# Kernel tuning notes

Measured on AMD Instinct MI355X. Metric: run time of the kernel, lower is better.

The kernel has to match this reference:

```python
import jax, jax.numpy as jnp
from jax import lax
import numpy as np

K = 2000      # self.k: entries kept per sample
T_SC = 3      # number of IHT iterations
DN = ('NCHW', 'OIHW', 'NCHW')


def keep_k_largest(X, k):
    # Per-sample hard threshold: keep the k largest-magnitude entries of the
    # flattened [C,H,W] activations, zero the rest (exactly k kept, as in argsort).
    B = X.shape[0]
    flat = X.reshape(B, -1)                                # [B, N]
    _, idx = lax.top_k(jnp.abs(flat), k)                   # [B, k]
    vals = jnp.take_along_axis(flat, idx, axis=1)          # [B, k]
    out = jnp.zeros_like(flat).at[jnp.arange(B)[:, None], idx].set(vals)
    return out.reshape(X.shape)


def _D_apply(X, W_D):
    # ConvTranspose2d(numb_atom -> dp_channels), stride 1, no padding:
    # full correlation with the spatially flipped, io-swapped kernel.
    kh, kw = W_D.shape[2], W_D.shape[3]
    Wt = jnp.flip(jnp.transpose(W_D, (1, 0, 2, 3)), (2, 3))  # [dp, atoms, kh, kw]
    return lax.conv_general_dilated(X, Wt, (1, 1),
                                    [(kh - 1, kh - 1), (kw - 1, kw - 1)],
                                    dimension_numbers=DN)


def _Dt_apply(Z, W_D):
    # Conv2d(dp_channels -> numb_atom) VALID; D_trans.weight = D.weight.permute(0,1,3,2)
    Wt = jnp.transpose(W_D, (0, 1, 3, 2))                  # [atoms, dp, kh, kw]
    return lax.conv_general_dilated(Z, Wt, (1, 1), 'VALID', dimension_numbers=DN)


def setup_inputs() -> dict:
    key = jax.random.key(0)
    k1, k2, k3 = jax.random.split(key, 3)
    Y = jax.random.normal(k1, (32, 3, 64, 64), jnp.float32)
    X0 = jax.random.normal(k2, (32, 128, 57, 57), jnp.float32)   # random init X in forward
    W_D = jax.random.normal(k3, (128, 3, 8, 8), jnp.float32) * 0.05
    return {"Y": Y, "X0": X0, "W_D": W_D}


def reference(Y, X0, W_D):
    # HT_arg = X - D_trans(D(X) - Y); then T_SC hard-threshold iterations.
    HT_arg = X0 - _Dt_apply(_D_apply(X0, W_D) - Y, W_D)
    X = HT_arg
    for i in range(T_SC):
        X = keep_k_largest(HT_arg, K)
        if i < T_SC - 1:  # final HT_arg update in the original is unused
            HT_arg = X - _Dt_apply(_D_apply(X, W_D) - Y, W_D)
    return X
```

## Files before the change

### kernel.cpp

```cpp
#include <hip/hip_runtime.h>

#define BATCH 32
#define ATOMS 128
#define CCH 3
#define XH 57
#define XW 57
#define OHH 64
#define OWW 64
#define KSEL 2000
#define PIX (XH*XW)
#define NPS (ATOMS*PIX)
#define NTOT (BATCH*NPS)
#define RPS (CCH*OHH*OWW)
#define RTOT (BATCH*RPS)
#define CANDCAP 32768
#define NW 24576
#define ZWORDS (32*2048 + 32*1024)

__global__ __launch_bounds__(256) void prep_k(const float* __restrict__ Wg,
    double* __restrict__ WDd, double* __restrict__ Wt2d,
    const float* __restrict__ Y, double* __restrict__ Rd,
    unsigned* __restrict__ zbuf) {
  int e = blockIdx.x * 256 + threadIdx.x;
  if (e < NW) {
    {
      int kw = e & 7; int t = e >> 3; int c = t % 3; t /= 3; int kh = t & 7; int a = t >> 3;
      WDd[e] = (double)Wg[(a*3 + c)*64 + kh*8 + kw];
    }
    {
      int a = e & 127; int t = e >> 7; int j = t & 7; int i = (t >> 3) & 7; int c = t >> 6;
      Wt2d[e] = (double)Wg[(a*3 + c)*64 + j*8 + i];
    }
  }
  if (e < RTOT) Rd[e] = -(double)Y[e];
  if (e < ZWORDS + 64) zbuf[e] = 0;
}

__global__ __launch_bounds__(256) void convD_k(const float* __restrict__ X,
    const double* __restrict__ WDd, double* __restrict__ Rd) {
  __shared__ double Xs[4][11][72];
  int p = blockIdx.x;
  int lg = (p & 7) * 256 + (p >> 3);
  int b = lg >> 6; int rem = lg & 63;
  int band = rem >> 2, quarter = rem & 3;
  int row0 = band * 4;
  int a_base = quarter * 32;
  int tid = threadIdx.x;
  int ox = tid & 63;
  int wv = __builtin_amdgcn_readfirstlane(tid >> 6);
  const float* Xb = X + (size_t)b * NPS;

  double acc[4][3];
#pragma unroll
  for (int ty = 0; ty < 4; ++ty)
#pragma unroll
    for (int c = 0; c < 3; ++c) acc[ty][c] = 0.0;

  for (int ch = 0; ch < 8; ++ch) {
    __syncthreads();
    for (int e = tid; e < 4 * 11 * 72; e += 256) {
      int ai = e / 792; int rem2 = e - ai * 792;
      int r = rem2 / 72; int ss = rem2 - r * 72;
      int gy = row0 - 7 + r;
      int xcol = ss - 7;
      int a = a_base + ch * 4 + ai;
      float v = 0.0f;
      if ((unsigned)xcol < (unsigned)XW && (unsigned)gy < (unsigned)XH)
        v = Xb[a * PIX + gy * XW + xcol];
      Xs[ai][r][ss] = (double)v;
    }
    __syncthreads();
    {
      int a = a_base + ch * 4 + wv;
      const double* Wa = WDd + a * 192;
#pragma unroll
      for (int r = 0; r < 11; ++r) {
        int gy = row0 - 7 + r;
        if ((unsigned)gy >= (unsigned)XH) continue;
        double xd[8];
#pragma unroll
        for (int t = 0; t < 8; ++t) xd[t] = Xs[wv][r][ox + t];
#pragma unroll
        for (int ty = 0; ty < 4; ++ty) {
          int kh = ty + 7 - r;
          if ((unsigned)kh < 8u) {
            const double* Wk = Wa + kh * 24;
#pragma unroll
            for (int kw = 0; kw < 8; ++kw) {
              acc[ty][0] = fma(xd[7 - kw], Wk[kw],      acc[ty][0]);
              acc[ty][1] = fma(xd[7 - kw], Wk[8 + kw],  acc[ty][1]);
              acc[ty][2] = fma(xd[7 - kw], Wk[16 + kw], acc[ty][2]);
            }
          }
        }
      }
    }
  }
#pragma unroll
  for (int ty = 0; ty < 4; ++ty) {
    int oy = row0 + ty;
#pragma unroll
    for (int c = 0; c < 3; ++c)
      atomicAdd(&Rd[((size_t)(b * CCH + c) << 12) + (oy << 6) + ox], acc[ty][c]);
  }
}

__global__ __launch_bounds__(256) void convD_sparse_k(const float* __restrict__ Wg,
    const int* __restrict__ nzidx, const float* __restrict__ nzval,
    const float* __restrict__ Y, float* __restrict__ R) {
  __shared__ double accd[512];
  __shared__ float Wf[8192];
  __shared__ int   li[KSEL];
  __shared__ float lv[KSEL];
  int p = blockIdx.x;
  int lg = (p & 7) * 96 + (p >> 3);
  int s = lg / 24; int r = lg % 24; int c = r >> 3; int band = r & 7;
  int row0 = band * 8;
  int tid = threadIdx.x;
  for (int e = tid; e < 512; e += 256) accd[e] = 0.0;
  for (int e = tid; e < 8192; e += 256) {
    int a = e >> 6, k2 = e & 63;
    Wf[e] = Wg[(a * 3 + c) * 64 + k2];
  }
  for (int e = tid; e < KSEL; e += 256) {
    li[e] = nzidx[s * KSEL + e];
    lv[e] = nzval[s * KSEL + e];
  }
  __syncthreads();
  int slot = tid >> 3, kw = tid & 7;
  for (int e = slot; e < KSEL; e += 32) {
    int idx = li[e];
    int a = (int)((unsigned)idx / 3249u);
    int pp = idx - a * 3249;
    int y = (int)((unsigned)pp / 57u);
    int x = pp - y * 57;
    int dy = y - row0;
    if (dy < -7 || dy > 7) continue;
    double val = (double)lv[e];
    const float* wp = Wf + (a << 6) + kw;
#pragma unroll
    for (int kh = 0; kh < 8; ++kh) {
      int rr = dy + kh;
      if ((unsigned)rr < 8u)
        __hip_atomic_fetch_add(&accd[(rr << 6) + x + kw],
                               val * (double)wp[kh << 3],
                               __ATOMIC_RELAXED, __HIP_MEMORY_SCOPE_WORKGROUP);
    }
  }
  __syncthreads();
  const float* Yb = Y + (((size_t)(s * CCH + c)) << 12) + (row0 << 6);
  float* Rb = R + (((size_t)(s * CCH + c)) << 12) + (row0 << 6);
  for (int e = tid; e < 512; e += 256)
    Rb[e] = (float)(accd[e] - (double)Yb[e]);
}

template <typename TR>
__global__ __launch_bounds__(256) void convDt_k(const TR* __restrict__ R,
    const double* __restrict__ Wt2d, const float* __restrict__ Xprev,
    float* __restrict__ HT, unsigned* __restrict__ g1) {
  __shared__ float Rl[3][15][72];
  __shared__ unsigned hh[1024];
  int p = blockIdx.x;
  int lg = (p & 7) * 512 + (p >> 3);
  int b = lg >> 7; int rem = lg & 127; int ag = rem >> 3; int by = rem & 7;
  int row0 = by * 8;
  int a0 = ag * 8;
  int tid = threadIdx.x;
  for (int e = tid; e < 1024; e += 256) hh[e] = 0;
  for (int e = tid; e < 3 * 15 * 72; e += 256) {
    int c = e / (15 * 72); int r2 = e - c * (15 * 72);
    int rr = r2 / 72; int cc = r2 - rr * 72;
    int gr = row0 + rr;
    float v = 0.0f;
    if (cc < OWW && gr < OHH)
      v = (float)R[((size_t)(b * CCH + c) << 12) + (gr << 6) + cc];
    Rl[c][rr][cc] = v;
  }
  __syncthreads();
  int x = tid & 63, yg = tid >> 6;
  int yb = yg * 2;
  double acc[8][2];
#pragma unroll
  for (int aa = 0; aa < 8; ++aa) { acc[aa][0] = 0.0; acc[aa][1] = 0.0; }

#pragma unroll 1
  for (int c = 0; c < 3; ++c) {
#pragma unroll 1
    for (int j = 0; j < 8; ++j) {
      double rw[9];
#pragma unroll
      for (int r = 0; r < 9; ++r) rw[r] = (double)Rl[c][yb + r][x + j];
#pragma unroll
      for (int i = 0; i < 8; ++i) {
        const double* wp = Wt2d + ((c * 8 + i) * 8 + j) * 128 + a0;
#pragma unroll
        for (int aa = 0; aa < 8; ++aa) {
          double w = wp[aa];
          acc[aa][0] = fma(rw[i + 0], w, acc[aa][0]);
          acc[aa][1] = fma(rw[i + 1], w, acc[aa][1]);
        }
      }
    }
  }
  if (x < XW) {
#pragma unroll
    for (int ty = 0; ty < 2; ++ty) {
      int yy = row0 + yb + ty;
      if (yy < XH) {
#pragma unroll
        for (int aa = 0; aa < 8; ++aa) {
          size_t xo = (size_t)(b * ATOMS + a0 + aa) * PIX + yy * XW + x;
          float fv = (float)((double)Xprev[xo] - acc[aa][ty]);
          HT[xo] = fv;
          unsigned u = __float_as_uint(fv) & 0x7fffffffu;
          unsigned bin = u >> 20;
          atomicAdd(&hh[bin >> 1], 1u << ((bin & 1) << 4));
        }
      }
    }
  }
  __syncthreads();
  unsigned* gp = g1 + (size_t)b * 2048;
  for (int e = tid; e < 1024; e += 256) {
    unsigned v = hh[e];
    unsigned lo = v & 0xffffu, hi = v >> 16;
    if (lo) atomicAdd(&gp[2 * e], lo);
    if (hi) atomicAdd(&gp[2 * e + 1], hi);
  }
}

__global__ __launch_bounds__(256) void histwrite_k(const float* __restrict__ HT,
    const unsigned* __restrict__ g1, unsigned* __restrict__ g2,
    int* __restrict__ cand, int* __restrict__ candcnt,
    float* __restrict__ Xo, int* __restrict__ nzidx, float* __restrict__ nzval,
    int* __restrict__ nzcnt, int emit) {
  __shared__ unsigned h[1024];
  __shared__ unsigned part[256];
  __shared__ int lidx[4096];
  __shared__ int kidx[2048];
  __shared__ float kval[2048];
  __shared__ int lcnt, lbase, kcnt, kbase, b1_sh;
  int tid = threadIdx.x;
  int s = blockIdx.x >> 5;
  int chunk = blockIdx.x & 31;
  const unsigned* hg1 = g1 + (size_t)s * 2048;
  unsigned psum = 0;
#pragma unroll
  for (int e = 0; e < 8; ++e) psum += hg1[tid * 8 + e];
  part[tid] = psum;
  for (int e = tid; e < 1024; e += 256) h[e] = 0;
  if (tid == 0) { lcnt = 0; kcnt = 0; }
  __syncthreads();
  if (tid == 0) {
    int Kv = KSEL;
    unsigned cumBefore = 0;
    int bsel = 0;
    for (int q = 255; q >= 0; --q) {
      unsigned ps = part[q];
      if ((int)(cumBefore + ps) >= Kv) {
        for (int e = q * 8 + 7;; --e) {
          unsigned c2 = cumBefore + hg1[e];
          if ((int)c2 >= Kv) { bsel = e; break; }
          cumBefore = c2;
        }
        break;
      }
      cumBefore += ps;
    }
    b1_sh = bsel;
  }
  __syncthreads();
  unsigned pre = (unsigned)b1_sh;
  size_t sbase = (size_t)s * NPS;
  const uint4* U4 = (const uint4*)(HT + sbase);
  float4* X4 = (float4*)(Xo + sbase);
  for (int i4 = chunk * 256 + tid; i4 < NPS / 4; i4 += 32 * 256) {
    uint4 v = U4[i4];
    unsigned uu[4] = {v.x, v.y, v.z, v.w};
    float oo[4];
#pragma unroll
    for (int t = 0; t < 4; ++t) {
      int il = i4 * 4 + t;
      unsigned u = uu[t] & 0x7fffffffu;
      unsigned bin = u >> 20;
      float val = __uint_as_float(uu[t]);
      if (bin > pre) {
        oo[t] = val;
        if (emit) {
          int pos = atomicAdd(&kcnt, 1);
          if (pos < 2048) { kidx[pos] = il; kval[pos] = val; }
        }
      } else if (bin < pre) {
        oo[t] = 0.0f;
      } else {
        oo[t] = val;
        atomicAdd(&h[(u >> 10) & 1023], 1u);
        int pos = atomicAdd(&lcnt, 1);
        if (pos < 4096) lidx[pos] = il;
      }
    }
    X4[i4] = make_float4(oo[0], oo[1], oo[2], oo[3]);
  }
  __syncthreads();
  if (tid == 0) {
    int n = lcnt < 4096 ? lcnt : 4096;
    lbase = atomicAdd(&candcnt[s], n);
    if (emit) {
      int kn = kcnt < 2048 ? kcnt : 2048;
      kbase = atomicAdd(&nzcnt[s], kn);
    }
  }
  __syncthreads();
  int n = lcnt < 4096 ? lcnt : 4096;
  for (int e = tid; e < n; e += 256) {
    int g = lbase + e;
    if (g < CANDCAP) cand[s * CANDCAP + g] = lidx[e];
  }
  if (emit) {
    int kn = kcnt < 2048 ? kcnt : 2048;
    for (int e = tid; e < kn; e += 256) {
      int g = kbase + e;
      if (g < KSEL) { nzidx[s * KSEL + g] = kidx[e]; nzval[s * KSEL + g] = kval[e]; }
    }
  }
  for (int e = tid; e < 1024; e += 256)
    if (h[e]) atomicAdd(&g2[s * 1024 + e], h[e]);
}

__global__ __launch_bounds__(256) void pass3_k(const float* __restrict__ HT,
    const int* __restrict__ cand, int* __restrict__ candcnt,
    unsigned* __restrict__ g1, unsigned* __restrict__ g2,
    float* __restrict__ Xo, int* __restrict__ nzidx, float* __restrict__ nzval,
    int* __restrict__ nzcnt, int emit) {
  int s = blockIdx.x;
  __shared__ unsigned h[1024];
  __shared__ unsigned part[256];
  __shared__ int eqidx[1024];
  __shared__ int kidx[2048];
  __shared__ float kval[2048];
  __shared__ int eqn, kcnt, kbase;
  __shared__ unsigned tau_sh;
  __shared__ int k3_sh, cutoff_sh;
  __shared__ int b1_sh, k1_sh, b2_sh, k2_sh;
  int t = threadIdx.x;
  unsigned* hg1 = g1 + (size_t)s * 2048;
  unsigned s1 = 0;
#pragma unroll
  for (int e = 0; e < 8; ++e) s1 += hg1[t * 8 + e];
  part[t] = s1;
  for (int e = t; e < 1024; e += 256) h[e] = 0;
  if (t == 0) { eqn = 0; kcnt = 0; }
  __syncthreads();
  if (t == 0) {
    int Kv = KSEL;
    unsigned cumBefore = 0;
    int bsel = 0;
    for (int q = 255; q >= 0; --q) {
      unsigned ps = part[q];
      if ((int)(cumBefore + ps) >= Kv) {
        for (int e = q * 8 + 7;; --e) {
          unsigned c2 = cumBefore + hg1[e];
          if ((int)c2 >= Kv) { bsel = e; break; }
          cumBefore = c2;
        }
        break;
      }
      cumBefore += ps;
    }
    b1_sh = bsel;
    k1_sh = Kv - (int)cumBefore;
  }
  __syncthreads();
  unsigned* hg = g2 + s * 1024;
  unsigned s2 = 0;
#pragma unroll
  for (int e = 0; e < 4; ++e) s2 += hg[t * 4 + e];
  part[t] = s2;
  __syncthreads();
  if (t == 0) {
    int Kv = k1_sh;
    unsigned cumBefore = 0;
    int bsel = 0;
    for (int q = 255; q >= 0; --q) {
      unsigned ps = part[q];
      if ((int)(cumBefore + ps) >= Kv) {
        for (int e = q * 4 + 3;; --e) {
          unsigned c2 = cumBefore + hg[e];
          if ((int)c2 >= Kv) { bsel = e; break; }
          cumBefore = c2;
        }
        break;
      }
      cumBefore += ps;
    }
    b2_sh = bsel;
    k2_sh = Kv - (int)cumBefore;
  }
  __syncthreads();
  int n = candcnt[s];
  if (n > CANDCAP) n = CANDCAP;
  unsigned pre21 = (((unsigned)b1_sh) << 10) | (unsigned)b2_sh;
  const unsigned* U = (const unsigned*)(HT + (size_t)s * NPS);
  for (int e = t; e < n; e += 256) {
    int i = cand[s * CANDCAP + e];
    unsigned u = U[i] & 0x7fffffffu;
    if ((u >> 10) == pre21) atomicAdd(&h[u & 1023], 1u);
  }
  __syncthreads();
  if (t == 0) {
    int Kv = k2_sh;
    unsigned cumBefore = 0;
    int b3 = 0;
    for (int e = 1023; e >= 0; --e) {
      unsigned c2 = cumBefore + h[e];
      if ((int)c2 >= Kv) { b3 = e; break; }
      cumBefore = c2;
    }
    tau_sh = (pre21 << 10) | (unsigned)b3;
    k3_sh = Kv - (int)cumBefore;
  }
  __syncthreads();
  unsigned tau = tau_sh;
  for (int e = t; e < n; e += 256) {
    int i = cand[s * CANDCAP + e];
    unsigned u = U[i] & 0x7fffffffu;
    if (u == tau) {
      int pos = atomicAdd(&eqn, 1);
      if (pos < 1024) eqidx[pos] = i;
    }
  }
  __syncthreads();
  if (t == 0) {
    int m = eqn < 1024 ? eqn : 1024;
    int k3 = k3_sh;
    int cutoff;
    if (k3 >= m) {
      cutoff = 0x7fffffff;
    } else {
      int last = -1;
      for (int r = 0; r < k3; ++r) {
        int mn = 0x7fffffff;
        for (int q = 0; q < m; ++q) {
          int v = eqidx[q];
          if (v > last && v < mn) mn = v;
        }
        last = mn;
      }
      cutoff = last;
    }
    cutoff_sh = cutoff;
  }
  __syncthreads();
  int co = cutoff_sh;
  float* Xs = Xo + (size_t)s * NPS;
  for (int e = t; e < n; e += 256) {
    int i = cand[s * CANDCAP + e];
    unsigned uval = U[i];
    unsigned u = uval & 0x7fffffffu;
    bool keep = (u > tau) || (u == tau && i <= co);
    float val = __uint_as_float(uval);
    Xs[i] = keep ? val : 0.0f;
    if (keep && emit) {
      int pos = atomicAdd(&kcnt, 1);
      if (pos < 2048) { kidx[pos] = i; kval[pos] = val; }
    }
  }
  __syncthreads();
  if (emit) {
    if (t == 0) {
      int kn = kcnt < 2048 ? kcnt : 2048;
      kbase = atomicAdd(&nzcnt[s], kn);
    }
    __syncthreads();
    int kn = kcnt < 2048 ? kcnt : 2048;
    for (int e = t; e < kn; e += 256) {
      int g = kbase + e;
      if (g < KSEL) { nzidx[s * KSEL + g] = kidx[e]; nzval[s * KSEL + g] = kval[e]; }
    }
  }
  __syncthreads();
  for (int e = t; e < 2048; e += 256) hg1[e] = 0;
  for (int e = t; e < 1024; e += 256) hg[e] = 0;
  if (t == 0) { candcnt[s] = 0; nzcnt[s] = 0; }
}

extern "C" void kernel_launch(void* const* d_in, const int* in_sizes, int n_in,
                              void* d_out, int out_size, void* d_ws, size_t ws_size,
                              hipStream_t stream) {
  const float* Y  = (const float*)d_in[0];
  const float* X0 = (const float*)d_in[1];
  const float* Wg = (const float*)d_in[2];
  float* Xout = (float*)d_out;

  double* WDd  = (double*)d_ws;
  double* Wt2d = WDd + NW;
  float* HT   = (float*)(Wt2d + NW);
  float* Rbuf = HT + NTOT;
  double* Rd  = (double*)(Rbuf + RTOT);
  unsigned* g1 = (unsigned*)(Rd + RTOT);
  unsigned* g2 = g1 + 32 * 2048;
  int* candcnt = (int*)(g2 + 32 * 1024);
  int* nzcnt = candcnt + 32;
  int* cand = nzcnt + 32;
  int* nzidx = cand + 32 * CANDCAP;
  float* nzval = (float*)(nzidx + 32 * KSEL);

  prep_k<<<dim3((RTOT + 255) / 256), dim3(256), 0, stream>>>(Wg, WDd, Wt2d, Y, Rd, g1);

  for (int it = 0; it < 3; ++it) {
    const float* Xsrc = (it == 0) ? X0 : (const float*)Xout;
    if (it == 0) {
      convD_k<<<dim3(2048), dim3(256), 0, stream>>>(Xsrc, WDd, Rd);
      convDt_k<double><<<dim3(4096), dim3(256), 0, stream>>>(Rd, Wt2d, Xsrc, HT, g1);
    } else {
      convD_sparse_k<<<dim3(BATCH * CCH * 8), dim3(256), 0, stream>>>(
          Wg, nzidx, nzval, Y, Rbuf);
      convDt_k<float><<<dim3(4096), dim3(256), 0, stream>>>(Rbuf, Wt2d, Xsrc, HT, g1);
    }
    int emit = (it < 2) ? 1 : 0;
    histwrite_k<<<dim3(BATCH * 32), dim3(256), 0, stream>>>(
        HT, g1, g2, cand, candcnt, Xout, nzidx, nzval, nzcnt, emit);
    pass3_k<<<dim3(BATCH), dim3(256), 0, stream>>>(
        HT, cand, candcnt, g1, g2, Xout, nzidx, nzval, nzcnt, emit);
  }
}
```

Measured before the change: 944.0 us.

## Run the transposed convolution on FP64 MFMA with a runtime lane-layout probe

Replaces the scalar FP64 FMA implementation of the D-transpose convolution with an implicit GEMM built on the 16x16x4 FP64 MFMA instruction. Each block handles one output row, four waves each cover 16 output columns, and the K dimension of 192 (channels x kernel taps) is stepped in groups of four. A one-wave probe kernel runs at startup and discovers the MFMA operand and result lane mapping at runtime, writing lookup tables that the main kernel uses. If the probe cannot validate the mapping, the kernel falls back to a slow scalar path. The aim is to move the dominant FP64 arithmetic onto the matrix cores, at the cost of an extra launch, table lookups and staging R in shared memory as doubles.

```diff
diff --git a/kernel.cpp b/kernel.cpp
--- a/kernel.cpp
+++ b/kernel.cpp
@@ -17,6 +17,9 @@
 #define NW 24576
 #define ZWORDS (32*2048 + 32*1024)
 
+typedef double f64x4 __attribute__((ext_vector_type(4)));
+typedef unsigned long long u64;
+
 __global__ __launch_bounds__(256) void prep_k(const float* __restrict__ Wg,
     double* __restrict__ WDd, double* __restrict__ Wt2d,
     const float* __restrict__ Y, double* __restrict__ Rd,
@@ -34,6 +37,141 @@
   }
   if (e < RTOT) Rd[e] = -(double)Y[e];
   if (e < ZWORDS + 64) zbuf[e] = 0;
+}
+
+__global__ __launch_bounds__(64) void mfprobe_k(double* __restrict__ prg,
+                                                int* __restrict__ tabs) {
+  int lane = threadIdx.x;
+  for (int i = 0; i < 64; ++i) {
+    double aval = (lane == i) ? 1.0 : 0.0;
+    double bval = (double)(lane + 1);
+    f64x4 acc = {0.0, 0.0, 0.0, 0.0};
+    acc = __builtin_amdgcn_mfma_f64_16x16x4f64(aval, bval, acc, 0, 0, 0);
+#pragma unroll
+    for (int r = 0; r < 4; ++r) prg[(i * 64 + lane) * 4 + r] = acc[r];
+  }
+  __syncthreads();
+  __shared__ u64 ssupp[64][4];
+  __shared__ u64 sbm[64];
+  __shared__ int mrow[64], kcls[64];
+  __shared__ int reps[16];
+  __shared__ int classmem[16][4];
+  __shared__ u64 colsets[16];
+  __shared__ int posrow[256];
+  __shared__ int pn[256];
+  __shared__ int okflag;
+  {
+    u64 m[4] = {0, 0, 0, 0}, bm = 0;
+    for (int p2 = 0; p2 < 256; ++p2) {
+      double v = prg[lane * 256 + p2];
+      if (v != 0.0) {
+        int b = (int)v - 1;
+        if (b >= 0 && b < 64) bm |= (1ull << b);
+        m[p2 >> 6] |= (1ull << (p2 & 63));
+      }
+    }
+#pragma unroll
+    for (int q = 0; q < 4; ++q) ssupp[lane][q] = m[q];
+    sbm[lane] = bm;
+  }
+  __syncthreads();
+  if (lane == 0) {
+    int nrows = 0, nks = 0;
+    u64 krep[4];
+    for (int i = 0; i < 64; ++i) {
+      int c = -1;
+      for (int q = 0; q < nrows && q < 16; ++q) {
+        int rp = reps[q];
+        if (ssupp[i][0] == ssupp[rp][0] && ssupp[i][1] == ssupp[rp][1] &&
+            ssupp[i][2] == ssupp[rp][2] && ssupp[i][3] == ssupp[rp][3]) { c = q; break; }
+      }
+      if (c < 0) { c = nrows; if (nrows < 16) reps[nrows] = i; nrows++; }
+      mrow[i] = c < 16 ? c : 0;
+      int kc = -1;
+      for (int q = 0; q < nks && q < 4; ++q) if (sbm[i] == krep[q]) { kc = q; break; }
+      if (kc < 0) { kc = nks; if (nks < 4) krep[nks] = sbm[i]; nks++; }
+      kcls[i] = kc < 4 ? kc : 0;
+    }
+    for (int c = 0; c < 16; ++c)
+      for (int q = 0; q < 4; ++q) classmem[c][q] = -1;
+    for (int i = 0; i < 64; ++i) classmem[mrow[i]][kcls[i]] = i;
+    for (int p2 = 0; p2 < 256; ++p2) posrow[p2] = -1;
+    for (int c = 0; c < nrows && c < 16; ++c) {
+      int rp = reps[c];
+      for (int p2 = 0; p2 < 256; ++p2)
+        if ((ssupp[rp][p2 >> 6] >> (p2 & 63)) & 1) posrow[p2] = c;
+    }
+    int nc = 0;
+    for (int p2 = 0; p2 < 256; ++p2) {
+      if (posrow[p2] == 0) {
+        u64 cs = 0;
+        for (int q = 0; q < 4; ++q) {
+          int i = classmem[0][q];
+          if (i >= 0) {
+            double v = prg[i * 256 + p2];
+            if (v != 0.0) cs |= (1ull << ((int)v - 1));
+          }
+        }
+        if (nc < 16) colsets[nc] = cs;
+        nc++;
+      }
+    }
+    okflag = (nrows == 16 && nks == 4 && nc == 16) ? 1 : 0;
+  }
+  __syncthreads();
+  for (int r = 0; r < 4; ++r) {
+    int p2 = lane * 4 + r;
+    int c = posrow[p2];
+    int n = -1;
+    if (c >= 0) {
+      u64 cs = 0;
+      for (int q = 0; q < 4; ++q) {
+        int i = classmem[c][q];
+        if (i >= 0) {
+          double v = prg[i * 256 + p2];
+          if (v != 0.0) cs |= (1ull << ((int)v - 1));
+        }
+      }
+      for (int q = 0; q < 16; ++q) if (colsets[q] == cs) { n = q; break; }
+    }
+    pn[p2] = n;
+  }
+  __syncthreads();
+  int bk = -1, bn = -1;
+  for (int i = 0; i < 64; ++i)
+    if ((sbm[i] >> lane) & 1) { bk = kcls[i]; break; }
+  for (int q = 0; q < 16; ++q)
+    if ((colsets[q] >> lane) & 1) { bn = q; break; }
+  {
+    double aval = (double)(mrow[lane] * 4 + kcls[lane] + 1);
+    double bval = (bk >= 0 && bn >= 0) ? (double)(bk * 16 + bn + 3) : 0.0;
+    f64x4 acc = {0.0, 0.0, 0.0, 0.0};
+    acc = __builtin_amdgcn_mfma_f64_16x16x4f64(aval, bval, acc, 0, 0, 0);
+    bool ok = (bk >= 0 && bn >= 0);
+#pragma unroll
+    for (int r = 0; r < 4; ++r) {
+      int p2 = lane * 4 + r;
+      int m = posrow[p2], n = pn[p2];
+      if (m < 0 || n < 0) { ok = false; continue; }
+      double ref = 0.0;
+      for (int k = 0; k < 4; ++k)
+        ref += (double)(m * 4 + k + 1) * (double)(k * 16 + n + 3);
+      if (acc[r] != ref) ok = false;
+    }
+    u64 vote = __ballot(ok);
+    if (lane == 0 && vote != ~0ull) okflag = 0;
+  }
+  __syncthreads();
+  tabs[lane]       = mrow[lane];
+  tabs[64 + lane]  = kcls[lane];
+  tabs[128 + lane] = bk;
+  tabs[192 + lane] = bn;
+#pragma unroll
+  for (int r = 0; r < 4; ++r) {
+    tabs[256 + lane * 4 + r] = posrow[lane * 4 + r];
+    tabs[512 + lane * 4 + r] = pn[lane * 4 + r];
+  }
+  if (lane == 0) tabs[768] = okflag;
 }
 
 __global__ __launch_bounds__(256) void convD_k(const float* __restrict__ X,
@@ -155,68 +293,89 @@
 }
 
 template <typename TR>
-__global__ __launch_bounds__(256) void convDt_k(const TR* __restrict__ R,
+__global__ __launch_bounds__(256) void convDtMM_k(const TR* __restrict__ R,
     const double* __restrict__ Wt2d, const float* __restrict__ Xprev,
-    float* __restrict__ HT, unsigned* __restrict__ g1) {
-  __shared__ float Rl[3][15][72];
+    float* __restrict__ HT, unsigned* __restrict__ g1,
+    const int* __restrict__ tabs) {
+  __shared__ double Rl[3][8][72];
   __shared__ unsigned hh[1024];
   int p = blockIdx.x;
-  int lg = (p & 7) * 512 + (p >> 3);
-  int b = lg >> 7; int rem = lg & 127; int ag = rem >> 3; int by = rem & 7;
-  int row0 = by * 8;
-  int a0 = ag * 8;
+  int lg = (p & 7) * 228 + (p >> 3);
+  int b = lg / 57;
+  int y = lg - b * 57;
   int tid = threadIdx.x;
+  int lane = tid & 63;
+  int wv = tid >> 6;
+  int x0 = wv * 16;
   for (int e = tid; e < 1024; e += 256) hh[e] = 0;
-  for (int e = tid; e < 3 * 15 * 72; e += 256) {
-    int c = e / (15 * 72); int r2 = e - c * (15 * 72);
+  for (int e = tid; e < 3 * 8 * 72; e += 256) {
+    int c = e / (8 * 72); int r2 = e - c * (8 * 72);
     int rr = r2 / 72; int cc = r2 - rr * 72;
-    int gr = row0 + rr;
-    float v = 0.0f;
-    if (cc < OWW && gr < OHH)
-      v = (float)R[((size_t)(b * CCH + c) << 12) + (gr << 6) + cc];
+    double v = 0.0;
+    if (cc < OWW)
+      v = (double)R[((size_t)(b * CCH + c) << 12) + ((y + rr) << 6) + cc];
     Rl[c][rr][cc] = v;
   }
-  __syncthreads();
-  int x = tid & 63, yg = tid >> 6;
-  int yb = yg * 2;
-  double acc[8][2];
-#pragma unroll
-  for (int aa = 0; aa < 8; ++aa) { acc[aa][0] = 0.0; acc[aa][1] = 0.0; }
-
-#pragma unroll 1
-  for (int c = 0; c < 3; ++c) {
-#pragma unroll 1
-    for (int j = 0; j < 8; ++j) {
-      double rw[9];
-#pragma unroll
-      for (int r = 0; r < 9; ++r) rw[r] = (double)Rl[c][yb + r][x + j];
-#pragma unroll
-      for (int i = 0; i < 8; ++i) {
-        const double* wp = Wt2d + ((c * 8 + i) * 8 + j) * 128 + a0;
-#pragma unroll
-        for (int aa = 0; aa < 8; ++aa) {
-          double w = wp[aa];
-          acc[aa][0] = fma(rw[i + 0], w, acc[aa][0]);
-          acc[aa][1] = fma(rw[i + 1], w, acc[aa][1]);
-        }
-      }
-    }
-  }
-  if (x < XW) {
-#pragma unroll
-    for (int ty = 0; ty < 2; ++ty) {
-      int yy = row0 + yb + ty;
-      if (yy < XH) {
-#pragma unroll
-        for (int aa = 0; aa < 8; ++aa) {
-          size_t xo = (size_t)(b * ATOMS + a0 + aa) * PIX + yy * XW + x;
-          float fv = (float)((double)Xprev[xo] - acc[aa][ty]);
+  int am = tabs[lane], ak = tabs[64 + lane];
+  int bk = tabs[128 + lane], bn = tabs[192 + lane];
+  int dm[4], dn[4];
+#pragma unroll
+  for (int r = 0; r < 4; ++r) {
+    dm[r] = tabs[256 + lane * 4 + r];
+    dn[r] = tabs[512 + lane * 4 + r];
+  }
+  int ok = tabs[768];
+  __syncthreads();
+
+  if (ok) {
+    f64x4 acc[8];
+#pragma unroll
+    for (int m = 0; m < 8; ++m) acc[m] = (f64x4){0.0, 0.0, 0.0, 0.0};
+    const double* Wa = Wt2d + (size_t)ak * 128 + am;
+    int bcol = x0 + bn;
+#pragma unroll 4
+    for (int step = 0; step < 48; ++step) {
+      int kg = step * 4 + bk;
+      int c = kg >> 6, i = (kg >> 3) & 7, j = kg & 7;
+      double bval = Rl[c][i][bcol + j];
+      const double* wp = Wa + (size_t)step * 512;
+#pragma unroll
+      for (int m = 0; m < 8; ++m)
+        acc[m] = __builtin_amdgcn_mfma_f64_16x16x4f64(wp[m * 16], bval,
+                                                      acc[m], 0, 0, 0);
+    }
+    int pixbase = y * XW;
+#pragma unroll
+    for (int m = 0; m < 8; ++m) {
+#pragma unroll
+      for (int r = 0; r < 4; ++r) {
+        int x = x0 + dn[r];
+        if (x < XW) {
+          int a = m * 16 + dm[r];
+          size_t xo = ((size_t)(b * ATOMS + a)) * PIX + pixbase + x;
+          float fv = (float)((double)Xprev[xo] - acc[m][r]);
           HT[xo] = fv;
           unsigned u = __float_as_uint(fv) & 0x7fffffffu;
           unsigned bin = u >> 20;
           atomicAdd(&hh[bin >> 1], 1u << ((bin & 1) << 4));
         }
       }
+    }
+  } else {
+    for (int idx = tid; idx < 128 * 64; idx += 256) {
+      int a = idx >> 6, x = idx & 63;
+      if (x >= XW) continue;
+      double acc = 0.0;
+      for (int kg = 0; kg < 192; ++kg) {
+        int c = kg >> 6, i = (kg >> 3) & 7, j = kg & 7;
+        acc = fma(Rl[c][i][x + j], Wt2d[(size_t)kg * 128 + a], acc);
+      }
+      size_t xo = ((size_t)(b * ATOMS + a)) * PIX + y * XW + x;
+      float fv = (float)((double)Xprev[xo] - acc);
+      HT[xo] = fv;
+      unsigned u = __float_as_uint(fv) & 0x7fffffffu;
+      unsigned bin = u >> 20;
+      atomicAdd(&hh[bin >> 1], 1u << ((bin & 1) << 4));
     }
   }
   __syncthreads();
@@ -504,18 +663,23 @@
   int* cand = nzcnt + 32;
   int* nzidx = cand + 32 * CANDCAP;
   float* nzval = (float*)(nzidx + 32 * KSEL);
+  double* prg = (double*)(nzval + 32 * KSEL);
+  int* tabs = (int*)(prg + 64 * 64 * 4);
 
   prep_k<<<dim3((RTOT + 255) / 256), dim3(256), 0, stream>>>(Wg, WDd, Wt2d, Y, Rd, g1);
+  mfprobe_k<<<dim3(1), dim3(64), 0, stream>>>(prg, tabs);
 
   for (int it = 0; it < 3; ++it) {
     const float* Xsrc = (it == 0) ? X0 : (const float*)Xout;
     if (it == 0) {
       convD_k<<<dim3(2048), dim3(256), 0, stream>>>(Xsrc, WDd, Rd);
-      convDt_k<double><<<dim3(4096), dim3(256), 0, stream>>>(Rd, Wt2d, Xsrc, HT, g1);
+      convDtMM_k<double><<<dim3(1824), dim3(256), 0, stream>>>(
+          Rd, Wt2d, Xsrc, HT, g1, tabs);
     } else {
       convD_sparse_k<<<dim3(BATCH * CCH * 8), dim3(256), 0, stream>>>(
           Wg, nzidx, nzval, Y, Rbuf);
-      convDt_k<float><<<dim3(4096), dim3(256), 0, stream>>>(Rbuf, Wt2d, Xsrc, HT, g1);
+      convDtMM_k<float><<<dim3(1824), dim3(256), 0, stream>>>(
+          Rbuf, Wt2d, Xsrc, HT, g1, tabs);
     }
     int emit = (it < 2) ? 1 : 0;
     histwrite_k<<<dim3(BATCH * 32), dim3(256), 0, stream>>>(
```

New measurement: 1.336 ms. +41.5%, slower.

## Compute dense transposed conv in fp32, recompute top-k candidates in fp64

Applied to the files above, without the earlier changes.

The dense Dt convolution now accumulates in float instead of double, which should cut FP64 arithmetic and register pressure in the heaviest kernel. To keep the top-k selection exact, the candidate set is widened to the coarse bin and one bin below. A new recompute kernel then re-evaluates each candidate in fp64, looking up the previous sparse X through a shared-memory hash, and builds a fresh histogram. pass3 selects from these recomputed values rather than HT. This adds a kernel launch and a per-candidate gather, and relies on fp32 error staying within one histogram bin.

```diff
diff --git a/kernel.cpp b/kernel.cpp
--- a/kernel.cpp
+++ b/kernel.cpp
@@ -15,10 +15,10 @@
 #define RTOT (BATCH*RPS)
 #define CANDCAP 32768
 #define NW 24576
-#define ZWORDS (32*2048 + 32*1024)
+#define ZWORDS (32*2048*2 + 32)
 
 __global__ __launch_bounds__(256) void prep_k(const float* __restrict__ Wg,
-    double* __restrict__ WDd, double* __restrict__ Wt2d,
+    double* __restrict__ WDd, float* __restrict__ Wt2f,
     const float* __restrict__ Y, double* __restrict__ Rd,
     unsigned* __restrict__ zbuf) {
   int e = blockIdx.x * 256 + threadIdx.x;
@@ -29,11 +29,11 @@
     }
     {
       int a = e & 127; int t = e >> 7; int j = t & 7; int i = (t >> 3) & 7; int c = t >> 6;
-      Wt2d[e] = (double)Wg[(a*3 + c)*64 + j*8 + i];
+      Wt2f[e] = Wg[(a*3 + c)*64 + j*8 + i];
     }
   }
   if (e < RTOT) Rd[e] = -(double)Y[e];
-  if (e < ZWORDS + 64) zbuf[e] = 0;
+  if (e < ZWORDS) zbuf[e] = 0;
 }
 
 __global__ __launch_bounds__(256) void convD_k(const float* __restrict__ X,
@@ -156,7 +156,7 @@
 
 template <typename TR>
 __global__ __launch_bounds__(256) void convDt_k(const TR* __restrict__ R,
-    const double* __restrict__ Wt2d, const float* __restrict__ Xprev,
+    const float* __restrict__ Wt2f, const float* __restrict__ Xprev,
     float* __restrict__ HT, unsigned* __restrict__ g1) {
   __shared__ float Rl[3][15][72];
   __shared__ unsigned hh[1024];
@@ -179,25 +179,25 @@
   __syncthreads();
   int x = tid & 63, yg = tid >> 6;
   int yb = yg * 2;
-  double acc[8][2];
-#pragma unroll
-  for (int aa = 0; aa < 8; ++aa) { acc[aa][0] = 0.0; acc[aa][1] = 0.0; }
+  float acc[8][2];
+#pragma unroll
+  for (int aa = 0; aa < 8; ++aa) { acc[aa][0] = 0.0f; acc[aa][1] = 0.0f; }
 
 #pragma unroll 1
   for (int c = 0; c < 3; ++c) {
 #pragma unroll 1
     for (int j = 0; j < 8; ++j) {
-      double rw[9];
-#pragma unroll
-      for (int r = 0; r < 9; ++r) rw[r] = (double)Rl[c][yb + r][x + j];
+      float rw[9];
+#pragma unroll
+      for (int r = 0; r < 9; ++r) rw[r] = Rl[c][yb + r][x + j];
 #pragma unroll
       for (int i = 0; i < 8; ++i) {
-        const double* wp = Wt2d + ((c * 8 + i) * 8 + j) * 128 + a0;
+        const float* wp = Wt2f + ((c * 8 + i) * 8 + j) * 128 + a0;
 #pragma unroll
         for (int aa = 0; aa < 8; ++aa) {
-          double w = wp[aa];
-          acc[aa][0] = fma(rw[i + 0], w, acc[aa][0]);
-          acc[aa][1] = fma(rw[i + 1], w, acc[aa][1]);
+          float w = wp[aa];
+          acc[aa][0] = fmaf(rw[i + 0], w, acc[aa][0]);
+          acc[aa][1] = fmaf(rw[i + 1], w, acc[aa][1]);
         }
       }
     }
@@ -210,7 +210,7 @@
 #pragma unroll
         for (int aa = 0; aa < 8; ++aa) {
           size_t xo = (size_t)(b * ATOMS + a0 + aa) * PIX + yy * XW + x;
-          float fv = (float)((double)Xprev[xo] - acc[aa][ty]);
+          float fv = Xprev[xo] - acc[aa][ty];
           HT[xo] = fv;
           unsigned u = __float_as_uint(fv) & 0x7fffffffu;
           unsigned bin = u >> 20;
@@ -230,16 +230,11 @@
 }
 
 __global__ __launch_bounds__(256) void histwrite_k(const float* __restrict__ HT,
-    const unsigned* __restrict__ g1, unsigned* __restrict__ g2,
-    int* __restrict__ cand, int* __restrict__ candcnt,
-    float* __restrict__ Xo, int* __restrict__ nzidx, float* __restrict__ nzval,
-    int* __restrict__ nzcnt, int emit) {
-  __shared__ unsigned h[1024];
+    const unsigned* __restrict__ g1, int* __restrict__ cand,
+    int* __restrict__ candcnt, float* __restrict__ Xo) {
   __shared__ unsigned part[256];
   __shared__ int lidx[4096];
-  __shared__ int kidx[2048];
-  __shared__ float kval[2048];
-  __shared__ int lcnt, lbase, kcnt, kbase, b1_sh;
+  __shared__ int lcnt, lbase, b1_sh;
   int tid = threadIdx.x;
   int s = blockIdx.x >> 5;
   int chunk = blockIdx.x & 31;
@@ -248,8 +243,7 @@
 #pragma unroll
   for (int e = 0; e < 8; ++e) psum += hg1[tid * 8 + e];
   part[tid] = psum;
-  for (int e = tid; e < 1024; e += 256) h[e] = 0;
-  if (tid == 0) { lcnt = 0; kcnt = 0; }
+  if (tid == 0) lcnt = 0;
   __syncthreads();
   if (tid == 0) {
     int Kv = KSEL;
@@ -270,7 +264,7 @@
     b1_sh = bsel;
   }
   __syncthreads();
-  unsigned pre = (unsigned)b1_sh;
+  unsigned blo = (unsigned)(b1_sh > 0 ? b1_sh - 1 : 0);
   size_t sbase = (size_t)s * NPS;
   const uint4* U4 = (const uint4*)(HT + sbase);
   float4* X4 = (float4*)(Xo + sbase);
@@ -283,20 +277,12 @@
       int il = i4 * 4 + t;
       unsigned u = uu[t] & 0x7fffffffu;
       unsigned bin = u >> 20;
-      float val = __uint_as_float(uu[t]);
-      if (bin > pre) {
-        oo[t] = val;
-        if (emit) {
-          int pos = atomicAdd(&kcnt, 1);
-          if (pos < 2048) { kidx[pos] = il; kval[pos] = val; }
-        }
-      } else if (bin < pre) {
-        oo[t] = 0.0f;
-      } else {
-        oo[t] = val;
-        atomicAdd(&h[(u >> 10) & 1023], 1u);
+      if (bin >= blo) {
+        oo[t] = __uint_as_float(uu[t]);
         int pos = atomicAdd(&lcnt, 1);
         if (pos < 4096) lidx[pos] = il;
+      } else {
+        oo[t] = 0.0f;
       }
     }
     X4[i4] = make_float4(oo[0], oo[1], oo[2], oo[3]);
@@ -305,10 +291,6 @@
   if (tid == 0) {
     int n = lcnt < 4096 ? lcnt : 4096;
     lbase = atomicAdd(&candcnt[s], n);
-    if (emit) {
-      int kn = kcnt < 2048 ? kcnt : 2048;
-      kbase = atomicAdd(&nzcnt[s], kn);
-    }
   }
   __syncthreads();
   int n = lcnt < 4096 ? lcnt : 4096;
@@ -316,37 +298,99 @@
     int g = lbase + e;
     if (g < CANDCAP) cand[s * CANDCAP + g] = lidx[e];
   }
-  if (emit) {
-    int kn = kcnt < 2048 ? kcnt : 2048;
-    for (int e = tid; e < kn; e += 256) {
-      int g = kbase + e;
-      if (g < KSEL) { nzidx[s * KSEL + g] = kidx[e]; nzval[s * KSEL + g] = kval[e]; }
-    }
-  }
-  for (int e = tid; e < 1024; e += 256)
-    if (h[e]) atomicAdd(&g2[s * 1024 + e], h[e]);
-}
-
-__global__ __launch_bounds__(256) void pass3_k(const float* __restrict__ HT,
-    const int* __restrict__ cand, int* __restrict__ candcnt,
-    unsigned* __restrict__ g1, unsigned* __restrict__ g2,
+}
+
+template <typename TR, bool SPX>
+__global__ __launch_bounds__(256) void recompute_k(const TR* __restrict__ R,
+    const float* __restrict__ Wt2f, const float* __restrict__ X0,
+    const int* __restrict__ pnzidx, const float* __restrict__ pnzval,
+    const int* __restrict__ cand, const int* __restrict__ candcnt,
+    float* __restrict__ candval, unsigned* __restrict__ g1x) {
+  __shared__ int hidx[4096];
+  __shared__ float hval[4096];
+  __shared__ unsigned hx[2048];
+  int s = blockIdx.x >> 3;
+  int chunk = blockIdx.x & 7;
+  int tid = threadIdx.x;
+  for (int e = tid; e < 2048; e += 256) hx[e] = 0;
+  if constexpr (SPX) {
+    for (int e = tid; e < 4096; e += 256) hidx[e] = -1;
+    __syncthreads();
+    for (int e = tid; e < KSEL; e += 256) {
+      int idx = pnzidx[s * KSEL + e];
+      float v = pnzval[s * KSEL + e];
+      int slot = idx & 4095;
+      while (true) {
+        int old = atomicCAS(&hidx[slot], -1, idx);
+        if (old == -1) { hval[slot] = v; break; }
+        slot = (slot + 1) & 4095;
+      }
+    }
+  }
+  __syncthreads();
+  int n = candcnt[s];
+  if (n > CANDCAP) n = CANDCAP;
+  const TR* Rb = R + ((size_t)(s * 3) << 12);
+  for (int e = chunk * 256 + tid; e < n; e += 2048) {
+    int i = cand[s * CANDCAP + e];
+    int a = (int)((unsigned)i / 3249u);
+    int p = i - a * 3249;
+    int y = (int)((unsigned)p / 57u);
+    int x = p - y * 57;
+    double xprev;
+    if constexpr (SPX) {
+      xprev = 0.0;
+      int slot = i & 4095;
+      while (true) {
+        int h = hidx[slot];
+        if (h == i) { xprev = (double)hval[slot]; break; }
+        if (h == -1) break;
+        slot = (slot + 1) & 4095;
+      }
+    } else {
+      xprev = (double)X0[(size_t)s * NPS + i];
+    }
+    double acc = 0.0;
+    for (int c = 0; c < 3; ++c) {
+#pragma unroll
+      for (int ii = 0; ii < 8; ++ii) {
+        const TR* rrow = Rb + (c << 12) + ((y + ii) << 6) + x;
+        const float* wrow = Wt2f + ((c * 8 + ii) * 8) * 128 + a;
+#pragma unroll
+        for (int jj = 0; jj < 8; ++jj)
+          acc = fma((double)rrow[jj], (double)wrow[jj * 128], acc);
+      }
+    }
+    float cf = (float)(xprev - acc);
+    candval[s * CANDCAP + e] = cf;
+    unsigned u = __float_as_uint(cf) & 0x7fffffffu;
+    atomicAdd(&hx[u >> 20], 1u);
+  }
+  __syncthreads();
+  unsigned* gp = g1x + (size_t)s * 2048;
+  for (int e = tid; e < 2048; e += 256)
+    if (hx[e]) atomicAdd(&gp[e], hx[e]);
+}
+
+__global__ __launch_bounds__(256) void pass3_k(const int* __restrict__ cand,
+    int* __restrict__ candcnt, const float* __restrict__ candval,
+    unsigned* __restrict__ g1, unsigned* __restrict__ g1x,
     float* __restrict__ Xo, int* __restrict__ nzidx, float* __restrict__ nzval,
-    int* __restrict__ nzcnt, int emit) {
+    int emit) {
   int s = blockIdx.x;
   __shared__ unsigned h[1024];
   __shared__ unsigned part[256];
   __shared__ int eqidx[1024];
   __shared__ int kidx[2048];
   __shared__ float kval[2048];
-  __shared__ int eqn, kcnt, kbase;
+  __shared__ int eqn, kcnt;
   __shared__ unsigned tau_sh;
-  __shared__ int k3_sh, cutoff_sh;
-  __shared__ int b1_sh, k1_sh, b2_sh, k2_sh;
+  __shared__ int k3_sh, cutoff_sh, b1_sh, k1_sh, b2_sh, k2_sh;
   int t = threadIdx.x;
-  unsigned* hg1 = g1 + (size_t)s * 2048;
+  unsigned* hx = g1x + (size_t)s * 2048;
   unsigned s1 = 0;
 #pragma unroll
-  for (int e = 0; e < 8; ++e) s1 += hg1[t * 8 + e];
+  for (int e = 0; e < 8; ++e) s1 += hx[t * 8 + e];
   part[t] = s1;
   for (int e = t; e < 1024; e += 256) h[e] = 0;
   if (t == 0) { eqn = 0; kcnt = 0; }
@@ -359,7 +403,7 @@
       unsigned ps = part[q];
       if ((int)(cumBefore + ps) >= Kv) {
         for (int e = q * 8 + 7;; --e) {
-          unsigned c2 = cumBefore + hg1[e];
+          unsigned c2 = cumBefore + hx[e];
           if ((int)c2 >= Kv) { bsel = e; break; }
           cumBefore = c2;
         }
@@ -368,14 +412,20 @@
       cumBefore += ps;
     }
     b1_sh = bsel;
-    k1_sh = Kv - (int)cumBefore;
-  }
-  __syncthreads();
-  unsigned* hg = g2 + s * 1024;
-  unsigned s2 = 0;
-#pragma unroll
-  for (int e = 0; e < 4; ++e) s2 += hg[t * 4 + e];
-  part[t] = s2;
+    k1_sh = KSEL - (int)cumBefore;
+  }
+  __syncthreads();
+  int n = candcnt[s];
+  if (n > CANDCAP) n = CANDCAP;
+  const int* cs = cand + s * CANDCAP;
+  const float* cv = candval + s * CANDCAP;
+  unsigned b1x = (unsigned)b1_sh;
+  for (int e = t; e < n; e += 256) {
+    unsigned u = __float_as_uint(cv[e]) & 0x7fffffffu;
+    if ((u >> 20) == b1x) atomicAdd(&h[(u >> 10) & 1023], 1u);
+  }
+  __syncthreads();
+  part[t] = h[t * 4] + h[t * 4 + 1] + h[t * 4 + 2] + h[t * 4 + 3];
   __syncthreads();
   if (t == 0) {
     int Kv = k1_sh;
@@ -385,7 +435,7 @@
       unsigned ps = part[q];
       if ((int)(cumBefore + ps) >= Kv) {
         for (int e = q * 4 + 3;; --e) {
-          unsigned c2 = cumBefore + hg[e];
+          unsigned c2 = cumBefore + h[e];
           if ((int)c2 >= Kv) { bsel = e; break; }
           cumBefore = c2;
         }
@@ -397,13 +447,11 @@
     k2_sh = Kv - (int)cumBefore;
   }
   __syncthreads();
-  int n = candcnt[s];
-  if (n > CANDCAP) n = CANDCAP;
-  unsigned pre21 = (((unsigned)b1_sh) << 10) | (unsigned)b2_sh;
-  const unsigned* U = (const unsigned*)(HT + (size_t)s * NPS);
+  for (int e = t; e < 1024; e += 256) h[e] = 0;
+  __syncthreads();
+  unsigned pre21 = (b1x << 10) | (unsigned)b2_sh;
   for (int e = t; e < n; e += 256) {
-    int i = cand[s * CANDCAP + e];
-    unsigned u = U[i] & 0x7fffffffu;
+    unsigned u = __float_as_uint(cv[e]) & 0x7fffffffu;
     if ((u >> 10) == pre21) atomicAdd(&h[u & 1023], 1u);
   }
   __syncthreads();
@@ -422,11 +470,10 @@
   __syncthreads();
   unsigned tau = tau_sh;
   for (int e = t; e < n; e += 256) {
-    int i = cand[s * CANDCAP + e];
-    unsigned u = U[i] & 0x7fffffffu;
+    unsigned u = __float_as_uint(cv[e]) & 0x7fffffffu;
     if (u == tau) {
       int pos = atomicAdd(&eqn, 1);
-      if (pos < 1024) eqidx[pos] = i;
+      if (pos < 1024) eqidx[pos] = cs[e];
     }
   }
   __syncthreads();
@@ -454,34 +501,27 @@
   int co = cutoff_sh;
   float* Xs = Xo + (size_t)s * NPS;
   for (int e = t; e < n; e += 256) {
-    int i = cand[s * CANDCAP + e];
-    unsigned uval = U[i];
-    unsigned u = uval & 0x7fffffffu;
+    int i = cs[e];
+    float cf = cv[e];
+    unsigned u = __float_as_uint(cf) & 0x7fffffffu;
     bool keep = (u > tau) || (u == tau && i <= co);
-    float val = __uint_as_float(uval);
-    Xs[i] = keep ? val : 0.0f;
+    Xs[i] = keep ? cf : 0.0f;
     if (keep && emit) {
       int pos = atomicAdd(&kcnt, 1);
-      if (pos < 2048) { kidx[pos] = i; kval[pos] = val; }
+      if (pos < 2048) { kidx[pos] = i; kval[pos] = cf; }
     }
   }
   __syncthreads();
   if (emit) {
-    if (t == 0) {
-      int kn = kcnt < 2048 ? kcnt : 2048;
-      kbase = atomicAdd(&nzcnt[s], kn);
-    }
-    __syncthreads();
-    int kn = kcnt < 2048 ? kcnt : 2048;
+    int kn = kcnt < KSEL ? kcnt : KSEL;
     for (int e = t; e < kn; e += 256) {
-      int g = kbase + e;
-      if (g < KSEL) { nzidx[s * KSEL + g] = kidx[e]; nzval[s * KSEL + g] = kval[e]; }
-    }
-  }
-  __syncthreads();
-  for (int e = t; e < 2048; e += 256) hg1[e] = 0;
-  for (int e = t; e < 1024; e += 256) hg[e] = 0;
-  if (t == 0) { candcnt[s] = 0; nzcnt[s] = 0; }
+      nzidx[s * KSEL + e] = kidx[e];
+      nzval[s * KSEL + e] = kval[e];
+    }
+  }
+  unsigned* hg1 = g1 + (size_t)s * 2048;
+  for (int e = t; e < 2048; e += 256) { hg1[e] = 0; hx[e] = 0; }
+  if (t == 0) candcnt[s] = 0;
 }
 
 extern "C" void kernel_launch(void* const* d_in, const int* in_sizes, int n_in,
@@ -493,34 +533,41 @@
   float* Xout = (float*)d_out;
 
   double* WDd  = (double*)d_ws;
-  double* Wt2d = WDd + NW;
-  float* HT   = (float*)(Wt2d + NW);
+  float* Wt2f  = (float*)(WDd + NW);
+  float* HT   = Wt2f + NW;
   float* Rbuf = HT + NTOT;
   double* Rd  = (double*)(Rbuf + RTOT);
   unsigned* g1 = (unsigned*)(Rd + RTOT);
-  unsigned* g2 = g1 + 32 * 2048;
-  int* candcnt = (int*)(g2 + 32 * 1024);
-  int* nzcnt = candcnt + 32;
-  int* cand = nzcnt + 32;
-  int* nzidx = cand + 32 * CANDCAP;
+  unsigned* g1x = g1 + 32 * 2048;
+  int* candcnt = (int*)(g1x + 32 * 2048);
+  int* cand = candcnt + 32;
+  float* candval = (float*)(cand + 32 * CANDCAP);
+  int* nzidx = (int*)(candval + 32 * CANDCAP);
   float* nzval = (float*)(nzidx + 32 * KSEL);
 
-  prep_k<<<dim3((RTOT + 255) / 256), dim3(256), 0, stream>>>(Wg, WDd, Wt2d, Y, Rd, g1);
+  prep_k<<<dim3((RTOT + 255) / 256), dim3(256), 0, stream>>>(Wg, WDd, Wt2f, Y, Rd, g1);
 
   for (int it = 0; it < 3; ++it) {
-    const float* Xsrc = (it == 0) ? X0 : (const float*)Xout;
     if (it == 0) {
-      convD_k<<<dim3(2048), dim3(256), 0, stream>>>(Xsrc, WDd, Rd);
-      convDt_k<double><<<dim3(4096), dim3(256), 0, stream>>>(Rd, Wt2d, Xsrc, HT, g1);
+      convD_k<<<dim3(2048), dim3(256), 0, stream>>>(X0, WDd, Rd);
+      convDt_k<double><<<dim3(4096), dim3(256), 0, stream>>>(Rd, Wt2f, X0, HT, g1);
     } else {
       convD_sparse_k<<<dim3(BATCH * CCH * 8), dim3(256), 0, stream>>>(
           Wg, nzidx, nzval, Y, Rbuf);
-      convDt_k<float><<<dim3(4096), dim3(256), 0, stream>>>(Rbuf, Wt2d, Xsrc, HT, g1);
+      convDt_k<float><<<dim3(4096), dim3(256), 0, stream>>>(Rbuf, Wt2f,
+          (const float*)Xout, HT, g1);
+    }
+    histwrite_k<<<dim3(BATCH * 32), dim3(256), 0, stream>>>(
+        HT, g1, cand, candcnt, Xout);
+    if (it == 0) {
+      recompute_k<double, false><<<dim3(BATCH * 8), dim3(256), 0, stream>>>(
+          Rd, Wt2f, X0, nullptr, nullptr, cand, candcnt, candval, g1x);
+    } else {
+      recompute_k<float, true><<<dim3(BATCH * 8), dim3(256), 0, stream>>>(
+          Rbuf, Wt2f, X0, nzidx, nzval, cand, candcnt, candval, g1x);
     }
     int emit = (it < 2) ? 1 : 0;
-    histwrite_k<<<dim3(BATCH * 32), dim3(256), 0, stream>>>(
-        HT, g1, g2, cand, candcnt, Xout, nzidx, nzval, nzcnt, emit);
     pass3_k<<<dim3(BATCH), dim3(256), 0, stream>>>(
-        HT, cand, candcnt, g1, g2, Xout, nzidx, nzval, nzcnt, emit);
-  }
-}
+        cand, candcnt, candval, g1, g1x, Xout, nzidx, nzval, emit);
+  }
+}
```

After: 1.108 ms. 1.17x slower.
